# Optimization experiments

Hardware: AMD Instinct MI355X
Metric: run time of the kernel (lower is better)

Reference implementation:

```python
import jax, jax.numpy as jnp
from jax import lax
import numpy as np

RADIUS = 1
DILATION = 2
NUM_BINS = 16  # DualSimilarityLoss uses num_bins=16
ALPHA = 5.0
BETA = 0.1
NOISE = 1e-4


def _avg_pool2(x):
    b, c, h, w = x.shape
    return x.reshape(b, c, h // 2, 2, w // 2, 2).mean(axis=(3, 5))


def _conv_rep(x, k, pad):
    # replicate-pad then VALID conv, NCHW / OIHW
    xp = jnp.pad(x, ((0, 0), (0, 0), (pad, pad), (pad, pad)), mode='edge')
    return lax.conv_general_dilated(xp, k, (1, 1), 'VALID',
                                    dimension_numbers=('NCHW', 'OIHW', 'NCHW'))


def _upsample_align_corners(x, H, W):
    # bilinear, align_corners=True (matches F.interpolate(..., align_corners=True))
    b, c, h, w = x.shape

    def coords(n_out, n_in):
        pos = jnp.arange(n_out, dtype=x.dtype) * ((n_in - 1) / (n_out - 1))
        i0 = jnp.clip(jnp.floor(pos).astype(jnp.int32), 0, n_in - 2)
        return i0, pos - i0.astype(x.dtype)

    y0, fy = coords(H, h)
    x0, fx = coords(W, w)
    rows = x[:, :, y0, :] * (1.0 - fy)[None, None, :, None] \
         + x[:, :, y0 + 1, :] * fy[None, None, :, None]
    out = rows[:, :, :, x0] * (1.0 - fx) + rows[:, :, :, x0 + 1] * fx
    return out


def _compute_mind(img, key):
    B, _, H, W = img.shape
    img = _avg_pool2(img)                      # (B,1,H/2,W/2)
    img = img + NOISE * jax.random.normal(key, img.shape, img.dtype)
    h, w = img.shape[2], img.shape[3]
    pad = RADIUS * DILATION                    # 2
    k = 2 * RADIUS + 1                         # 3
    ones_k = jnp.ones((1, 1, k, k), img.dtype)
    padded = jnp.pad(img, ((0, 0), (0, 0), (pad, pad), (pad, pad)), mode='edge')
    patch_mean = lax.conv_general_dilated(padded, ones_k, (1, 1), 'VALID',
                                          dimension_numbers=('NCHW', 'OIHW', 'NCHW')) / (k * k)
    patch_mean = jnp.pad(patch_mean, ((0, 0), (0, 0), (pad, pad), (pad, pad)), mode='edge')
    c = pad
    center = padded[:, :, c:c + h, c:c + w]
    variance = (center - patch_mean[:, :, c:c + h, c:c + w]) ** 2
    variance = _conv_rep(variance, ones_k, RADIUS) / (k * k)
    variance = jnp.maximum(variance, 1e-4)
    descs = []
    for i in range(-RADIUS, RADIUS + 1):
        for j in range(-RADIUS, RADIUS + 1):
            if i == 0 and j == 0:
                continue
            dx, dy = i * DILATION, j * DILATION
            off = padded[:, :, c + dy:c + dy + h, c + dx:c + dx + w]
            diff = jnp.clip((center - off) ** 2 / (variance * 2 + 1e-6), 0.0, 50.0)
            descs.append(diff)
    m = jnp.exp(-jnp.concatenate(descs, axis=1))          # (B,8,h,w)
    m = m / (m.sum(axis=1, keepdims=True) + 1e-8)
    m = jnp.where(jnp.isnan(m), 0.0, m)
    if (h, w) != (H, W):
        m = _upsample_align_corners(m, H, W)
    return m


def _nmi_loss(x, y, kx, ky):
    B = x.shape[0]
    x = x[:, :, ::2, ::2]
    y = y[:, :, ::2, ::2]
    x = x + NOISE * jax.random.normal(kx, x.shape, x.dtype)
    y = y + NOISE * jax.random.normal(ky, y.shape, y.dtype)
    xf = jnp.clip((x.reshape(B, -1) + 1.0) / 2.0, 0.001, 0.999)
    yf = jnp.clip((y.reshape(B, -1) + 1.0) / 2.0, 0.001, 0.999)
    grid = jnp.linspace(0.0, 1.0, NUM_BINS + 1)
    xb = jnp.clip(jnp.searchsorted(grid, xf, side='left') - 1, 0, NUM_BINS - 1)
    yb = jnp.clip(jnp.searchsorted(grid, yf, side='left') - 1, 0, NUM_BINS - 1)
    idx = xb * NUM_BINS + yb                               # (B,N)
    hist = jnp.zeros((B, NUM_BINS * NUM_BINS), jnp.float32)
    hist = hist.at[jnp.arange(B)[:, None], idx].add(1.0)
    hist = hist.reshape(B, NUM_BINS, NUM_BINS)
    hist = hist / (hist.sum(axis=(1, 2), keepdims=True) + 1e-10)
    xh = hist.sum(axis=2)
    yh = hist.sum(axis=1)
    eps = 1e-5
    hist = hist + eps
    xh = xh + eps
    yh = yh + eps
    mi = jnp.sum(hist * (jnp.log(hist) - jnp.log(xh[:, :, None] * yh[:, None, :])), axis=(1, 2))
    hx = -jnp.sum(xh * jnp.log(xh), axis=1)
    hy = -jnp.sum(yh * jnp.log(yh), axis=1)
    se = hx + hy
    nmi = jnp.where(se < 1e-10, 0.0, 2.0 * mi / se)
    nmi = jnp.clip(nmi, -1.0, 1.0)
    return -jnp.clip(nmi.mean(), -1.0, 1.0)


def _reg_loss(flow, ku, kv):
    sx = jnp.array([[-1, 0, 1], [-2, 0, 2], [-1, 0, 1]], jnp.float32).reshape(1, 1, 3, 3)
    sy = jnp.array([[-1, -2, -1], [0, 0, 0], [1, 2, 1]], jnp.float32).reshape(1, 1, 3, 3)
    lp = jnp.array([[0, 1, 0], [1, -4, 1], [0, 1, 0]], jnp.float32).reshape(1, 1, 3, 3)
    f = _avg_pool2(flow)
    u = f[:, 0:1] + NOISE * jax.random.normal(ku, f[:, 0:1].shape, f.dtype)
    v = f[:, 1:2] + NOISE * jax.random.normal(kv, f[:, 1:2].shape, f.dtype)
    grad_mag = _conv_rep(u, sx, 1) ** 2 + _conv_rep(u, sy, 1) ** 2 \
             + _conv_rep(v, sx, 1) ** 2 + _conv_rep(v, sy, 1) ** 2
    lap_mag = _conv_rep(u, lp, 1) ** 2 + _conv_rep(v, lp, 1) ** 2
    return jnp.clip(grad_mag, 0.0, 100.0).mean() + jnp.clip(lap_mag, 0.0, 100.0).mean()


def _total_loss(fixed, moved, flow):
    fixed = jnp.where(jnp.isnan(fixed), 0.0, fixed)
    moved = jnp.where(jnp.isnan(moved), 0.0, moved)
    flow = jnp.where(jnp.isnan(flow), 0.0, flow)
    ks = jax.random.split(jax.random.key(42), 6)
    mi = _nmi_loss(fixed, moved, ks[0], ks[1])
    mx = _compute_mind(fixed, ks[2])
    my = _compute_mind(moved, ks[3])
    d = jnp.abs(mx - my)
    mind = jnp.where(jnp.isnan(d), 0.0, d).mean()
    reg = _reg_loss(flow, ks[4], ks[5])
    return mi + ALPHA * mind + BETA * reg


def setup_inputs() -> dict:
    key = jax.random.key(0)
    k1, k2, k3 = jax.random.split(key, 3)
    B, H, W = 8, 512, 512
    return {
        'fixed': jax.random.normal(k1, (B, 1, H, W), jnp.float32),
        'moved': jax.random.normal(k2, (B, 1, H, W), jnp.float32),
        'flow': jax.random.normal(k3, (B, 2, H, W), jnp.float32),
    }


def reference(fixed, moved, flow):
    return _total_loss(fixed, moved, flow)
```

## Files before the change

### kernel.cpp

```cpp
#include <hip/hip_runtime.h>
#include <cmath>

#define BATCH 8
#define HF 512
#define WF 512
#define HS 256
#define WS 256
#define PLANE_S (HS * WS)
#define PLANE_F (HF * WF)

#define NMIND_BLOCKS 512
#define NREG_BLOCKS  128

#define OFF_HISTP 0
#define OFF_PMIND (512 * 1024)
#define OFF_PGRAD (OFF_PMIND + NMIND_BLOCKS * 8)
#define OFF_PLAP  (OFF_PGRAD + NREG_BLOCKS * 8)
#define OFF_NMI   (OFF_PLAP + NREG_BLOCKS * 8)

#define IMG_R 39
#define IMG_S 41
#define T_R 36
#define T_S 37
#define V_R 34
#define V_S 35

__device__ __forceinline__ int clampi(int v, int lo, int hi) {
    return v < lo ? lo : (v > hi ? hi : v);
}

__device__ __forceinline__ int bin_of(float x) {
    float v = (x + 1.0f) * 0.5f;
    v = fminf(fmaxf(v, 0.001f), 0.999f);
    float t = v * 16.0f;
    float ft = floorf(t);
    int c = (int)ft + ((t > ft) ? 1 : 0);
    int b = c - 1;
    return b < 0 ? 0 : (b > 15 ? 15 : b);
}

__global__ __launch_bounds__(256, 2) void mega_mind_kernel(
    const float* __restrict__ fixed, const float* __restrict__ moved,
    unsigned* __restrict__ hist_part, double* __restrict__ pmind)
{
    const float FS = (float)(255.0 / 511.0);
    int tx = blockIdx.x, ty = blockIdx.y, b = blockIdx.z;
    int Xb = tx * 64, Yb = ty * 64;
    int dbx = (int)((float)Xb * FS);
    int dby = (int)((float)Yb * FS);
    int ibx = dbx - 3, iby = dby - 3;

    __shared__ float S[15098];
    float* imgF = S;
    float* imgM = S + IMG_R * IMG_S;
    float* varF = S + 2 * IMG_R * IMG_S;
    float* varM = varF + V_R * V_S;
    float* diff = varM + V_R * V_S;
    float* tF   = diff;
    float* tM   = diff + T_R * T_S;
    __shared__ unsigned lh[256];
    __shared__ float red[256];

    int tid = threadIdx.x;
    lh[tid] = 0u;
    __syncthreads();

    const float* fb = fixed + (size_t)b * PLANE_F;
    const float* mb = moved + (size_t)b * PLANE_F;
    int oy0 = ty * 32, ox0 = tx * 32;
    for (int i = tid; i < IMG_R * IMG_R; i += 256) {
        int r = i / IMG_R, c = i - r * IMG_R;
        int gy = iby + r, gx = ibx + c;
        int cy = clampi(gy, 0, HS - 1), cx = clampi(gx, 0, WS - 1);
        const float* fp = fb + (size_t)(cy * 2) * WF + (size_t)(cx * 2);
        const float* mp = mb + (size_t)(cy * 2) * WF + (size_t)(cx * 2);
        float2 f0 = *(const float2*)fp;
        float2 f1 = *(const float2*)(fp + WF);
        float2 m0 = *(const float2*)mp;
        float2 m1 = *(const float2*)(mp + WF);
        imgF[r * IMG_S + c] = (f0.x + f0.y + f1.x + f1.y) * 0.25f;
        imgM[r * IMG_S + c] = (m0.x + m0.y + m1.x + m1.y) * 0.25f;
        if ((unsigned)(gy - oy0) < 32u && (unsigned)(gx - ox0) < 32u) {
            atomicAdd(&lh[bin_of(f0.x) * 16 + bin_of(m0.x)], 1u);
        }
    }
    __syncthreads();
    hist_part[((size_t)(b * 64 + ty * 8 + tx)) * 256 + tid] = lh[tid];

    for (int i = tid; i < T_R * T_R; i += 256) {
        int r = i / T_R, c = i - r * T_R;
        float sF = 0.f, sM = 0.f;
        #pragma unroll
        for (int dy = 0; dy < 3; dy++)
            #pragma unroll
            for (int dx = 0; dx < 3; dx++) {
                sF += imgF[(r + dy) * IMG_S + c + dx];
                sM += imgM[(r + dy) * IMG_S + c + dx];
            }
        float dF = imgF[(r + 2) * IMG_S + c + 2] - sF / 9.0f;
        float dM = imgM[(r + 2) * IMG_S + c + 2] - sM / 9.0f;
        tF[r * T_S + c] = dF * dF;
        tM[r * T_S + c] = dM * dM;
    }
    __syncthreads();

    for (int i = tid; i < V_R * V_R; i += 256) {
        int r = i / V_R, c = i - r * V_R;
        float sF = 0.f, sM = 0.f;
        #pragma unroll
        for (int dy = 0; dy < 3; dy++)
            #pragma unroll
            for (int dx = 0; dx < 3; dx++) {
                sF += tF[(r + dy) * T_S + c + dx];
                sM += tM[(r + dy) * T_S + c + dx];
            }
        varF[r * V_S + c] = fmaxf(sF / 9.0f, 1e-4f);
        varM[r * V_S + c] = fmaxf(sM / 9.0f, 1e-4f);
    }
    __syncthreads();

    for (int i = tid; i < V_R * V_R; i += 256) {
        int r = i / V_R, c = i - r * V_R;
        float cF = imgF[(r + 3) * IMG_S + c + 3];
        float cM = imgM[(r + 3) * IMG_S + c + 3];
        float dF2 = 2.f * varF[r * V_S + c] + 1e-6f;
        float dM2 = 2.f * varM[r * V_S + c] + 1e-6f;
        float eF[8], eM[8];
        float sF = 0.f, sM = 0.f;
        int ch = 0;
        #pragma unroll
        for (int ii = -1; ii <= 1; ii++) {
            #pragma unroll
            for (int jj = -1; jj <= 1; jj++) {
                if (ii == 0 && jj == 0) continue;
                float aF = cF - imgF[(r + 3 + 2 * jj) * IMG_S + (c + 3 + 2 * ii)];
                float aM = cM - imgM[(r + 3 + 2 * jj) * IMG_S + (c + 3 + 2 * ii)];
                float qF = fminf(aF * aF / dF2, 50.f);
                float qM = fminf(aM * aM / dM2, 50.f);
                float vF_ = expf(-qF), vM_ = expf(-qM);
                eF[ch] = vF_; eM[ch] = vM_;
                sF += vF_; sM += vM_;
                ch++;
            }
        }
        float wF = 1.f / (sF + 1e-8f);
        float wM = 1.f / (sM + 1e-8f);
        float* dp = diff + (size_t)(r * V_S + c) * 8;
        #pragma unroll
        for (int q = 0; q < 8; q++) dp[q] = eF[q] * wF - eM[q] * wM;
    }
    __syncthreads();

    float local = 0.f;
    for (int k = tid; k < 64 * 64; k += 256) {
        int dy = k >> 6, dx = k & 63;
        float py = (float)(Yb + dy) * FS;
        int y0 = (int)py; if (y0 > HS - 2) y0 = HS - 2;
        float fy = py - (float)y0;
        float px = (float)(Xb + dx) * FS;
        int x0 = (int)px; if (x0 > WS - 2) x0 = WS - 2;
        float fx = px - (float)x0;
        const float* p00 = diff + (size_t)((y0 - dby) * V_S + (x0 - dbx)) * 8;
        const float* p10 = p00 + V_S * 8;
        #pragma unroll
        for (int q = 0; q < 8; q++) {
            float a  = p00[q]     * (1.f - fy) + p10[q]     * fy;
            float c2 = p00[q + 8] * (1.f - fy) + p10[q + 8] * fy;
            local += fabsf(a * (1.f - fx) + c2 * fx);
        }
    }
    red[tid] = local;
    __syncthreads();
    for (int s = 128; s > 0; s >>= 1) { if (tid < s) red[tid] += red[tid + s]; __syncthreads(); }
    if (tid == 0) pmind[b * 64 + ty * 8 + tx] = (double)red[0];
}

#define RP 66
#define RS 67
__global__ __launch_bounds__(256, 2) void reg_fused_kernel(
    const float* __restrict__ flow, double* __restrict__ pgrad, double* __restrict__ plap)
{
    int tt = blockIdx.x;
    int b = blockIdx.y;
    int tyr = tt >> 2, txr = tt & 3;
    int y0p = tyr * 64, x0p = txr * 64;
    __shared__ float U[RP * RS], V[RP * RS];
    __shared__ float red[256];
    const float* ur = flow + (size_t)(b * 2) * PLANE_F;
    const float* vr = ur + PLANE_F;
    int tid = threadIdx.x;
    for (int i = tid; i < RP * RP; i += 256) {
        int r = i / RP, c = i - r * RP;
        int gy = clampi(y0p - 1 + r, 0, HS - 1);
        int gx = clampi(x0p - 1 + c, 0, WS - 1);
        const float* uu = ur + (size_t)(gy * 2) * WF + (size_t)(gx * 2);
        const float* vv = vr + (size_t)(gy * 2) * WF + (size_t)(gx * 2);
        float2 u0 = *(const float2*)uu, u1 = *(const float2*)(uu + WF);
        float2 v0 = *(const float2*)vv, v1 = *(const float2*)(vv + WF);
        U[r * RS + c] = (u0.x + u0.y + u1.x + u1.y) * 0.25f;
        V[r * RS + c] = (v0.x + v0.y + v1.x + v1.y) * 0.25f;
    }
    __syncthreads();
    float g = 0.f, l = 0.f;
    for (int k = tid; k < 64 * 64; k += 256) {
        int y = k >> 6, x = k & 63;
        const float* u0 = &U[y * RS + x];
        const float* v0 = &V[y * RS + x];
        float a00 = u0[0],      a01 = u0[1],          a02 = u0[2];
        float a10 = u0[RS],     a11 = u0[RS + 1],     a12 = u0[RS + 2];
        float a20 = u0[2 * RS], a21 = u0[2 * RS + 1], a22 = u0[2 * RS + 2];
        float c00 = v0[0],      c01 = v0[1],          c02 = v0[2];
        float c10 = v0[RS],     c11 = v0[RS + 1],     c12 = v0[RS + 2];
        float c20 = v0[2 * RS], c21 = v0[2 * RS + 1], c22 = v0[2 * RS + 2];
        float gxu = (a02 - a00) + 2.f * (a12 - a10) + (a22 - a20);
        float gyu = (a20 - a00) + 2.f * (a21 - a01) + (a22 - a02);
        float gxv = (c02 - c00) + 2.f * (c12 - c10) + (c22 - c20);
        float gyv = (c20 - c00) + 2.f * (c21 - c01) + (c22 - c02);
        float lpu = a01 + a10 - 4.f * a11 + a12 + a21;
        float lpv = c01 + c10 - 4.f * c11 + c12 + c21;
        float grad = gxu * gxu + gyu * gyu + gxv * gxv + gyv * gyv;
        float lap = lpu * lpu + lpv * lpv;
        g += fminf(grad, 100.f);
        l += fminf(lap, 100.f);
    }
    red[tid] = g;
    __syncthreads();
    for (int s = 128; s > 0; s >>= 1) { if (tid < s) red[tid] += red[tid + s]; __syncthreads(); }
    if (tid == 0) pgrad[b * 16 + tt] = (double)red[0];
    __syncthreads();
    red[tid] = l;
    __syncthreads();
    for (int s = 128; s > 0; s >>= 1) { if (tid < s) red[tid] += red[tid + s]; __syncthreads(); }
    if (tid == 0) plap[b * 16 + tt] = (double)red[0];
}

__global__ void nmi_kernel(const unsigned* __restrict__ hist_part, float* __restrict__ nmi_out) {
    int b = blockIdx.x;
    int t = threadIdx.x;
    __shared__ float p[256];
    __shared__ float xh[16], yh[16];
    __shared__ float red[256];
    unsigned hv = 0;
    const unsigned* hp = hist_part + (size_t)b * 64 * 256 + t;
    for (int i = 0; i < 64; i++) hv += hp[i * 256];
    float pv = (float)hv / 65536.0f;
    p[t] = pv;
    __syncthreads();
    if (t < 16) {
        float s = 0.f;
        for (int j = 0; j < 16; j++) s += p[t * 16 + j];
        xh[t] = s;
    } else if (t < 32) {
        int j = t - 16;
        float s = 0.f;
        for (int i = 0; i < 16; i++) s += p[i * 16 + j];
        yh[j] = s;
    }
    __syncthreads();
    const float eps = 1e-5f;
    int i = t >> 4, j = t & 15;
    float h = pv + eps;
    float mi_term = h * (logf(h) - logf((xh[i] + eps) * (yh[j] + eps)));
    red[t] = mi_term;
    __syncthreads();
    for (int s = 128; s > 0; s >>= 1) { if (t < s) red[t] += red[t + s]; __syncthreads(); }
    float mi = red[0];
    __syncthreads();
    float e_term = 0.f;
    if (t < 16) { float xe = xh[t] + eps; e_term = -xe * logf(xe); }
    else if (t < 32) { float ye = yh[t - 16] + eps; e_term = -ye * logf(ye); }
    red[t] = e_term;
    __syncthreads();
    for (int s = 128; s > 0; s >>= 1) { if (t < s) red[t] += red[t + s]; __syncthreads(); }
    if (t == 0) {
        float se = red[0];
        float nmi = (se < 1e-10f) ? 0.f : 2.f * mi / se;
        nmi_out[b] = fminf(fmaxf(nmi, -1.f), 1.f);
    }
}

__global__ void final_kernel(const float* __restrict__ nmi, const double* __restrict__ pmind,
                             const double* __restrict__ pgrad, const double* __restrict__ plap,
                             float* __restrict__ out) {
    __shared__ double red[256];
    int t = threadIdx.x;
    double sm = 0.0;
    for (int i = t; i < NMIND_BLOCKS; i += 256) sm += pmind[i];
    double sg = 0.0, sl = 0.0;
    for (int i = t; i < NREG_BLOCKS; i += 256) { sg += pgrad[i]; sl += plap[i]; }
    red[t] = sm;
    __syncthreads();
    for (int s = 128; s > 0; s >>= 1) { if (t < s) red[t] += red[t + s]; __syncthreads(); }
    double mind_sum = red[0];
    __syncthreads();
    red[t] = sg;
    __syncthreads();
    for (int s = 128; s > 0; s >>= 1) { if (t < s) red[t] += red[t + s]; __syncthreads(); }
    double grad_sum = red[0];
    __syncthreads();
    red[t] = sl;
    __syncthreads();
    for (int s = 128; s > 0; s >>= 1) { if (t < s) red[t] += red[t + s]; __syncthreads(); }
    double lap_sum = red[0];
    if (t == 0) {
        float s = 0.f;
        for (int b = 0; b < BATCH; b++) s += nmi[b];
        s /= (float)BATCH;
        s = fminf(fmaxf(s, -1.f), 1.f);
        double mi_loss = -(double)s;
        double mind_mean = mind_sum / (64.0 * (double)PLANE_F);
        double reg = grad_sum / (double)(BATCH * PLANE_S) + lap_sum / (double)(BATCH * PLANE_S);
        out[0] = (float)(mi_loss + 5.0 * mind_mean + 0.1 * reg);
    }
}

extern "C" void kernel_launch(void* const* d_in, const int* in_sizes, int n_in,
                              void* d_out, int out_size, void* d_ws, size_t ws_size,
                              hipStream_t stream) {
    const float* fixed = (const float*)d_in[0];
    const float* moved = (const float*)d_in[1];
    const float* flow  = (const float*)d_in[2];
    float* out = (float*)d_out;
    char* ws = (char*)d_ws;

    unsigned* hist_part = (unsigned*)(ws + OFF_HISTP);
    double*   pmind     = (double*)(ws + OFF_PMIND);
    double*   pgrad     = (double*)(ws + OFF_PGRAD);
    double*   plap      = (double*)(ws + OFF_PLAP);
    float*    nmi       = (float*)(ws + OFF_NMI);

    mega_mind_kernel<<<dim3(8, 8, 8), 256, 0, stream>>>(fixed, moved, hist_part, pmind);
    reg_fused_kernel<<<dim3(16, 8), 256, 0, stream>>>(flow, pgrad, plap);
    nmi_kernel<<<BATCH, 256, 0, stream>>>(hist_part, nmi);
    final_kernel<<<1, 256, 0, stream>>>(nmi, pmind, pgrad, plap, out);
}
```

Measured before the change: 115.9 us.

## Fuse MIND and regularization kernels into one launch with smaller tiles

Merges the MIND/histogram kernel and the flow regularization kernel into a single launch, using blockIdx.z to choose the branch. Output tiles shrink from 64x64 to 32x32, giving 2048 MIND blocks and 512 reg blocks with less shared memory each and launch bounds raised to 4 blocks per CU. The aim is better occupancy and load balance across CUs and one fewer kernel launch. In exchange, halo overhead per tile grows, there are 4x more partial histograms for nmi_kernel to sum, and divisions are replaced by reciprocal multiplies, which may shift float results slightly.

New measurement: 112.5 us. -3.0%, faster.

```diff
diff --git a/kernel.cpp b/kernel.cpp
--- a/kernel.cpp
+++ b/kernel.cpp
@@ -9,21 +9,24 @@
 #define PLANE_S (HS * WS)
 #define PLANE_F (HF * WF)
 
-#define NMIND_BLOCKS 512
-#define NREG_BLOCKS  128
+#define NMIND_BLOCKS 2048
+#define NREG_BLOCKS  512
 
 #define OFF_HISTP 0
-#define OFF_PMIND (512 * 1024)
+#define OFF_PMIND (2048 * 1024)
 #define OFF_PGRAD (OFF_PMIND + NMIND_BLOCKS * 8)
 #define OFF_PLAP  (OFF_PGRAD + NREG_BLOCKS * 8)
 #define OFF_NMI   (OFF_PLAP + NREG_BLOCKS * 8)
 
-#define IMG_R 39
-#define IMG_S 41
-#define T_R 36
-#define T_S 37
-#define V_R 34
-#define V_S 35
+#define IMG_R 23
+#define IMG_S 24
+#define T_R 20
+#define T_S 21
+#define V_R 18
+#define V_S 19
+
+#define RP 34
+#define RS 35
 
 __device__ __forceinline__ int clampi(int v, int lo, int hi) {
     return v < lo ? lo : (v > hi ? hi : v);
@@ -39,18 +42,78 @@
     return b < 0 ? 0 : (b > 15 ? 15 : b);
 }
 
-__global__ __launch_bounds__(256, 2) void mega_mind_kernel(
+__global__ __launch_bounds__(256, 4) void fused_main_kernel(
     const float* __restrict__ fixed, const float* __restrict__ moved,
-    unsigned* __restrict__ hist_part, double* __restrict__ pmind)
+    const float* __restrict__ flow,
+    unsigned* __restrict__ hist_part, double* __restrict__ pmind,
+    double* __restrict__ pgrad, double* __restrict__ plap)
 {
+    __shared__ float S[4524];
+    __shared__ unsigned lh[256];
+    __shared__ float red[256];
+    int tid = threadIdx.x;
+
+    if (blockIdx.z < 2) {
+        int idx = blockIdx.z * 256 + blockIdx.y * 16 + blockIdx.x;
+        int b = idx >> 6, t64 = idx & 63;
+        int y0p = (t64 >> 3) * 32, x0p = (t64 & 7) * 32;
+        float* U = S;
+        float* V = S + RP * RS;
+        const float* ur = flow + (size_t)(b * 2) * PLANE_F;
+        const float* vr = ur + PLANE_F;
+        for (int i = tid; i < RP * RP; i += 256) {
+            int r = i / RP, c = i - r * RP;
+            int gy = clampi(y0p - 1 + r, 0, HS - 1);
+            int gx = clampi(x0p - 1 + c, 0, WS - 1);
+            const float* uu = ur + (size_t)(gy * 2) * WF + (size_t)(gx * 2);
+            const float* vv = vr + (size_t)(gy * 2) * WF + (size_t)(gx * 2);
+            float2 u0 = *(const float2*)uu, u1 = *(const float2*)(uu + WF);
+            float2 v0 = *(const float2*)vv, v1 = *(const float2*)(vv + WF);
+            U[r * RS + c] = (u0.x + u0.y + u1.x + u1.y) * 0.25f;
+            V[r * RS + c] = (v0.x + v0.y + v1.x + v1.y) * 0.25f;
+        }
+        __syncthreads();
+        float g = 0.f, l = 0.f;
+        for (int k = tid; k < 32 * 32; k += 256) {
+            int y = k >> 5, x = k & 31;
+            const float* u0 = &U[y * RS + x];
+            const float* v0 = &V[y * RS + x];
+            float a00 = u0[0],      a01 = u0[1],          a02 = u0[2];
+            float a10 = u0[RS],     a11 = u0[RS + 1],     a12 = u0[RS + 2];
+            float a20 = u0[2 * RS], a21 = u0[2 * RS + 1], a22 = u0[2 * RS + 2];
+            float c00 = v0[0],      c01 = v0[1],          c02 = v0[2];
+            float c10 = v0[RS],     c11 = v0[RS + 1],     c12 = v0[RS + 2];
+            float c20 = v0[2 * RS], c21 = v0[2 * RS + 1], c22 = v0[2 * RS + 2];
+            float gxu = (a02 - a00) + 2.f * (a12 - a10) + (a22 - a20);
+            float gyu = (a20 - a00) + 2.f * (a21 - a01) + (a22 - a02);
+            float gxv = (c02 - c00) + 2.f * (c12 - c10) + (c22 - c20);
+            float gyv = (c20 - c00) + 2.f * (c21 - c01) + (c22 - c02);
+            float lpu = a01 + a10 - 4.f * a11 + a12 + a21;
+            float lpv = c01 + c10 - 4.f * c11 + c12 + c21;
+            float grad = gxu * gxu + gyu * gyu + gxv * gxv + gyv * gyv;
+            float lap = lpu * lpu + lpv * lpv;
+            g += fminf(grad, 100.f);
+            l += fminf(lap, 100.f);
+        }
+        red[tid] = g;
+        __syncthreads();
+        for (int s = 128; s > 0; s >>= 1) { if (tid < s) red[tid] += red[tid + s]; __syncthreads(); }
+        if (tid == 0) pgrad[b * 64 + t64] = (double)red[0];
+        __syncthreads();
+        red[tid] = l;
+        __syncthreads();
+        for (int s = 128; s > 0; s >>= 1) { if (tid < s) red[tid] += red[tid + s]; __syncthreads(); }
+        if (tid == 0) plap[b * 64 + t64] = (double)red[0];
+        return;
+    }
+
     const float FS = (float)(255.0 / 511.0);
-    int tx = blockIdx.x, ty = blockIdx.y, b = blockIdx.z;
-    int Xb = tx * 64, Yb = ty * 64;
+    int tx = blockIdx.x, ty = blockIdx.y, b = blockIdx.z - 2;
+    int Xb = tx * 32, Yb = ty * 32;
     int dbx = (int)((float)Xb * FS);
     int dby = (int)((float)Yb * FS);
     int ibx = dbx - 3, iby = dby - 3;
 
-    __shared__ float S[15098];
     float* imgF = S;
     float* imgM = S + IMG_R * IMG_S;
     float* varF = S + 2 * IMG_R * IMG_S;
@@ -58,16 +121,13 @@
     float* diff = varM + V_R * V_S;
     float* tF   = diff;
     float* tM   = diff + T_R * T_S;
-    __shared__ unsigned lh[256];
-    __shared__ float red[256];
-
-    int tid = threadIdx.x;
+
     lh[tid] = 0u;
     __syncthreads();
 
     const float* fb = fixed + (size_t)b * PLANE_F;
     const float* mb = moved + (size_t)b * PLANE_F;
-    int oy0 = ty * 32, ox0 = tx * 32;
+    int oy0 = ty * 16, ox0 = tx * 16;
     for (int i = tid; i < IMG_R * IMG_R; i += 256) {
         int r = i / IMG_R, c = i - r * IMG_R;
         int gy = iby + r, gx = ibx + c;
@@ -80,13 +140,14 @@
         float2 m1 = *(const float2*)(mp + WF);
         imgF[r * IMG_S + c] = (f0.x + f0.y + f1.x + f1.y) * 0.25f;
         imgM[r * IMG_S + c] = (m0.x + m0.y + m1.x + m1.y) * 0.25f;
-        if ((unsigned)(gy - oy0) < 32u && (unsigned)(gx - ox0) < 32u) {
+        if ((unsigned)(gy - oy0) < 16u && (unsigned)(gx - ox0) < 16u) {
             atomicAdd(&lh[bin_of(f0.x) * 16 + bin_of(m0.x)], 1u);
         }
     }
     __syncthreads();
-    hist_part[((size_t)(b * 64 + ty * 8 + tx)) * 256 + tid] = lh[tid];
-
+    hist_part[((size_t)(b * 256 + ty * 16 + tx)) * 256 + tid] = lh[tid];
+
+    const float NINTH = 1.0f / 9.0f;
     for (int i = tid; i < T_R * T_R; i += 256) {
         int r = i / T_R, c = i - r * T_R;
         float sF = 0.f, sM = 0.f;
@@ -97,8 +158,8 @@
                 sF += imgF[(r + dy) * IMG_S + c + dx];
                 sM += imgM[(r + dy) * IMG_S + c + dx];
             }
-        float dF = imgF[(r + 2) * IMG_S + c + 2] - sF / 9.0f;
-        float dM = imgM[(r + 2) * IMG_S + c + 2] - sM / 9.0f;
+        float dF = imgF[(r + 2) * IMG_S + c + 2] - sF * NINTH;
+        float dM = imgM[(r + 2) * IMG_S + c + 2] - sM * NINTH;
         tF[r * T_S + c] = dF * dF;
         tM[r * T_S + c] = dM * dM;
     }
@@ -114,8 +175,8 @@
                 sF += tF[(r + dy) * T_S + c + dx];
                 sM += tM[(r + dy) * T_S + c + dx];
             }
-        varF[r * V_S + c] = fmaxf(sF / 9.0f, 1e-4f);
-        varM[r * V_S + c] = fmaxf(sM / 9.0f, 1e-4f);
+        varF[r * V_S + c] = fmaxf(sF * NINTH, 1e-4f);
+        varM[r * V_S + c] = fmaxf(sM * NINTH, 1e-4f);
     }
     __syncthreads();
 
@@ -125,6 +186,8 @@
         float cM = imgM[(r + 3) * IMG_S + c + 3];
         float dF2 = 2.f * varF[r * V_S + c] + 1e-6f;
         float dM2 = 2.f * varM[r * V_S + c] + 1e-6f;
+        float invF = 1.0f / dF2;
+        float invM = 1.0f / dM2;
         float eF[8], eM[8];
         float sF = 0.f, sM = 0.f;
         int ch = 0;
@@ -135,8 +198,8 @@
                 if (ii == 0 && jj == 0) continue;
                 float aF = cF - imgF[(r + 3 + 2 * jj) * IMG_S + (c + 3 + 2 * ii)];
                 float aM = cM - imgM[(r + 3 + 2 * jj) * IMG_S + (c + 3 + 2 * ii)];
-                float qF = fminf(aF * aF / dF2, 50.f);
-                float qM = fminf(aM * aM / dM2, 50.f);
+                float qF = fminf(aF * aF * invF, 50.f);
+                float qM = fminf(aM * aM * invM, 50.f);
                 float vF_ = expf(-qF), vM_ = expf(-qM);
                 eF[ch] = vF_; eM[ch] = vM_;
                 sF += vF_; sM += vM_;
@@ -152,8 +215,8 @@
     __syncthreads();
 
     float local = 0.f;
-    for (int k = tid; k < 64 * 64; k += 256) {
-        int dy = k >> 6, dx = k & 63;
+    for (int k = tid; k < 32 * 32; k += 256) {
+        int dy = k >> 5, dx = k & 31;
         float py = (float)(Yb + dy) * FS;
         int y0 = (int)py; if (y0 > HS - 2) y0 = HS - 2;
         float fy = py - (float)y0;
@@ -172,66 +235,7 @@
     red[tid] = local;
     __syncthreads();
     for (int s = 128; s > 0; s >>= 1) { if (tid < s) red[tid] += red[tid + s]; __syncthreads(); }
-    if (tid == 0) pmind[b * 64 + ty * 8 + tx] = (double)red[0];
-}
-
-#define RP 66
-#define RS 67
-__global__ __launch_bounds__(256, 2) void reg_fused_kernel(
-    const float* __restrict__ flow, double* __restrict__ pgrad, double* __restrict__ plap)
-{
-    int tt = blockIdx.x;
-    int b = blockIdx.y;
-    int tyr = tt >> 2, txr = tt & 3;
-    int y0p = tyr * 64, x0p = txr * 64;
-    __shared__ float U[RP * RS], V[RP * RS];
-    __shared__ float red[256];
-    const float* ur = flow + (size_t)(b * 2) * PLANE_F;
-    const float* vr = ur + PLANE_F;
-    int tid = threadIdx.x;
-    for (int i = tid; i < RP * RP; i += 256) {
-        int r = i / RP, c = i - r * RP;
-        int gy = clampi(y0p - 1 + r, 0, HS - 1);
-        int gx = clampi(x0p - 1 + c, 0, WS - 1);
-        const float* uu = ur + (size_t)(gy * 2) * WF + (size_t)(gx * 2);
-        const float* vv = vr + (size_t)(gy * 2) * WF + (size_t)(gx * 2);
-        float2 u0 = *(const float2*)uu, u1 = *(const float2*)(uu + WF);
-        float2 v0 = *(const float2*)vv, v1 = *(const float2*)(vv + WF);
-        U[r * RS + c] = (u0.x + u0.y + u1.x + u1.y) * 0.25f;
-        V[r * RS + c] = (v0.x + v0.y + v1.x + v1.y) * 0.25f;
-    }
-    __syncthreads();
-    float g = 0.f, l = 0.f;
-    for (int k = tid; k < 64 * 64; k += 256) {
-        int y = k >> 6, x = k & 63;
-        const float* u0 = &U[y * RS + x];
-        const float* v0 = &V[y * RS + x];
-        float a00 = u0[0],      a01 = u0[1],          a02 = u0[2];
-        float a10 = u0[RS],     a11 = u0[RS + 1],     a12 = u0[RS + 2];
-        float a20 = u0[2 * RS], a21 = u0[2 * RS + 1], a22 = u0[2 * RS + 2];
-        float c00 = v0[0],      c01 = v0[1],          c02 = v0[2];
-        float c10 = v0[RS],     c11 = v0[RS + 1],     c12 = v0[RS + 2];
-        float c20 = v0[2 * RS], c21 = v0[2 * RS + 1], c22 = v0[2 * RS + 2];
-        float gxu = (a02 - a00) + 2.f * (a12 - a10) + (a22 - a20);
-        float gyu = (a20 - a00) + 2.f * (a21 - a01) + (a22 - a02);
-        float gxv = (c02 - c00) + 2.f * (c12 - c10) + (c22 - c20);
-        float gyv = (c20 - c00) + 2.f * (c21 - c01) + (c22 - c02);
-        float lpu = a01 + a10 - 4.f * a11 + a12 + a21;
-        float lpv = c01 + c10 - 4.f * c11 + c12 + c21;
-        float grad = gxu * gxu + gyu * gyu + gxv * gxv + gyv * gyv;
-        float lap = lpu * lpu + lpv * lpv;
-        g += fminf(grad, 100.f);
-        l += fminf(lap, 100.f);
-    }
-    red[tid] = g;
-    __syncthreads();
-    for (int s = 128; s > 0; s >>= 1) { if (tid < s) red[tid] += red[tid + s]; __syncthreads(); }
-    if (tid == 0) pgrad[b * 16 + tt] = (double)red[0];
-    __syncthreads();
-    red[tid] = l;
-    __syncthreads();
-    for (int s = 128; s > 0; s >>= 1) { if (tid < s) red[tid] += red[tid + s]; __syncthreads(); }
-    if (tid == 0) plap[b * 16 + tt] = (double)red[0];
+    if (tid == 0) pmind[b * 256 + ty * 16 + tx] = (double)red[0];
 }
 
 __global__ void nmi_kernel(const unsigned* __restrict__ hist_part, float* __restrict__ nmi_out) {
@@ -241,8 +245,8 @@
     __shared__ float xh[16], yh[16];
     __shared__ float red[256];
     unsigned hv = 0;
-    const unsigned* hp = hist_part + (size_t)b * 64 * 256 + t;
-    for (int i = 0; i < 64; i++) hv += hp[i * 256];
+    const unsigned* hp = hist_part + (size_t)b * 256 * 256 + t;
+    for (int i = 0; i < 256; i++) hv += hp[i * 256];
     float pv = (float)hv / 65536.0f;
     p[t] = pv;
     __syncthreads();
@@ -329,8 +333,8 @@
     double*   plap      = (double*)(ws + OFF_PLAP);
     float*    nmi       = (float*)(ws + OFF_NMI);
 
-    mega_mind_kernel<<<dim3(8, 8, 8), 256, 0, stream>>>(fixed, moved, hist_part, pmind);
-    reg_fused_kernel<<<dim3(16, 8), 256, 0, stream>>>(flow, pgrad, plap);
+    fused_main_kernel<<<dim3(16, 16, 10), 256, 0, stream>>>(fixed, moved, flow,
+                                                            hist_part, pmind, pgrad, plap);
     nmi_kernel<<<BATCH, 256, 0, stream>>>(hist_part, nmi);
     final_kernel<<<1, 256, 0, stream>>>(nmi, pmind, pgrad, plap, out);
 }
```
